# Kernel tuning notes

Hardware: AMD Instinct MI355X
Metric: run time of the kernel (lower is better)

The kernel has to match this reference:

```python
import jax, jax.numpy as jnp
import numpy as np

HIDDEN_DIM = 128
NUM_HEADS = 4
B, S = 16, 1024
NEG = -1e9
EPS = 1e-5


def setup_inputs() -> dict:
    key = jax.random.key(0)
    ks = jax.random.split(key, 6)
    D, H = HIDDEN_DIM, NUM_HEADS
    x = jax.random.normal(ks[0], (B, S, D), dtype=jnp.float32)
    edge_type_matrix = jax.random.randint(ks[1], (S, S), 0, 5, dtype=jnp.int64)
    scale = 0.02
    W_in = jax.random.normal(ks[2], (H, 3 * D, D), dtype=jnp.float32) * scale   # per-head in_proj_weight
    b_in = jax.random.normal(ks[3], (H, 3 * D), dtype=jnp.float32) * scale      # per-head in_proj_bias
    W_out = jax.random.normal(ks[4], (H, D, D), dtype=jnp.float32) * scale      # per-head out_proj.weight
    b_out = jax.random.normal(ks[5], (H, D), dtype=jnp.float32) * scale         # per-head out_proj.bias
    return {"x": x, "edge_type_matrix": edge_type_matrix,
            "W_in": W_in, "b_in": b_in, "W_out": W_out, "b_out": b_out}


def reference(x, edge_type_matrix, W_in, b_in, W_out, b_out):
    Bx, Sx, D = x.shape
    H = W_in.shape[0]
    # F.layer_norm(x, x.size()[1:]): normalize jointly over (S, D), no affine
    mu = jnp.mean(x, axis=(1, 2), keepdims=True)
    var = jnp.mean(jnp.square(x - mu), axis=(1, 2), keepdims=True)
    xn = (x - mu) / jnp.sqrt(var + EPS)
    # all heads' qkv in one contraction: [b,h,s,3D]
    qkv = jnp.einsum('bsd,hed->bhse', xn, W_in) + b_in[None, :, None, :]
    q, k, v = jnp.split(qkv, 3, axis=-1)                      # each [b,h,s,D]
    scores = jnp.einsum('bhsd,bhtd->bhst', q, k) / jnp.sqrt(jnp.float32(D))
    # additive mask per head: 0 where edge_type == head_id(1..H), else -1e9
    head_ids = jnp.arange(1, H + 1, dtype=edge_type_matrix.dtype)
    mask = jnp.where(edge_type_matrix[None, :, :] == head_ids[:, None, None],
                     jnp.float32(0.0), jnp.float32(NEG))       # [h,s,s]
    attn = jax.nn.softmax(scores + mask[None], axis=-1)
    ctx = jnp.einsum('bhst,bhtd->bhsd', attn, v)
    # torch out_proj: ctx @ W.T + b
    out_h = jnp.einsum('bhsd,hed->bhse', ctx, W_out) + b_out[None, :, None, :]
    # dropout p=0.05 is identity in eval mode; concat heads on feature dim
    out = jnp.transpose(out_h, (0, 2, 1, 3)).reshape(Bx, Sx, H * D)
    return out


if __name__ == '__main__':
    inp = setup_inputs()
    y = reference(**inp)
    print(y.shape)
```

## Files before the change

kernel.cpp:

```cpp
#include <hip/hip_runtime.h>
#include <math.h>

static constexpr int Dh = 128;
static constexpr int NH = 4;
static constexpr int NB = 16;
static constexpr int SS = 1024;
static constexpr float NEGF = -1e9f;
static constexpr float SCALE = 0.08838834764831843f;

typedef short s16x8 __attribute__((ext_vector_type(8)));
typedef short s16x4 __attribute__((ext_vector_type(4)));
typedef float f32x4 __attribute__((ext_vector_type(4)));

#define MFMA32(a, b, c) __builtin_amdgcn_mfma_f32_16x16x32_bf16(a, b, c, 0, 0, 0)
#define MFMA16(a, b, c) __builtin_amdgcn_mfma_f32_16x16x16bf16_1k(a, b, c, 0, 0, 0)

__device__ inline ushort f2bf(float f) {
    union { float f; unsigned u; } v; v.f = f;
    unsigned r = v.u + 0x7FFFu + ((v.u >> 16) & 1u);
    return (ushort)(r >> 16);
}

__global__ __launch_bounds__(256) void ln_mask_kernel(const float* __restrict__ x,
                                                      float* __restrict__ part,
                                                      const int* __restrict__ edge,
                                                      unsigned long long* __restrict__ mbit) {
    const int b = blockIdx.x >> 4, p = blockIdx.x & 15;
    const int tid = threadIdx.x;
    const float4* xb = (const float4*)(x + (size_t)b * SS * Dh) + p * 2048;
    float s = 0.f, ss = 0.f;
    for (int i = tid; i < 2048; i += 256) {
        float4 v = xb[i];
        s  += v.x + v.y + v.z + v.w;
        ss += v.x * v.x + v.y * v.y + v.z * v.z + v.w * v.w;
    }
    __shared__ float r1[256], r2[256];
    r1[tid] = s; r2[tid] = ss;
    __syncthreads();
    for (int off = 128; off > 0; off >>= 1) {
        if (tid < off) { r1[tid] += r1[tid + off]; r2[tid] += r2[tid + off]; }
        __syncthreads();
    }
    if (tid == 0) { part[blockIdx.x * 2] = r1[0]; part[blockIdx.x * 2 + 1] = r2[0]; }

    if (blockIdx.x < 64) {
        const int idx = blockIdx.x * 256 + tid;
        const int sr = idx >> 4, w = idx & 15;
        const int4* ep = (const int4*)(edge + (size_t)sr * SS + w * 64);
        unsigned long long m0 = 0, m1 = 0, m2 = 0, m3 = 0;
        #pragma unroll
        for (int j = 0; j < 16; ++j) {
            int4 e = ep[j];
            const int base = j * 4;
            m0 |= (e.x == 1) ? (1ull << (base + 0)) : 0ull;
            m1 |= (e.x == 2) ? (1ull << (base + 0)) : 0ull;
            m2 |= (e.x == 3) ? (1ull << (base + 0)) : 0ull;
            m3 |= (e.x == 4) ? (1ull << (base + 0)) : 0ull;
            m0 |= (e.y == 1) ? (1ull << (base + 1)) : 0ull;
            m1 |= (e.y == 2) ? (1ull << (base + 1)) : 0ull;
            m2 |= (e.y == 3) ? (1ull << (base + 1)) : 0ull;
            m3 |= (e.y == 4) ? (1ull << (base + 1)) : 0ull;
            m0 |= (e.z == 1) ? (1ull << (base + 2)) : 0ull;
            m1 |= (e.z == 2) ? (1ull << (base + 2)) : 0ull;
            m2 |= (e.z == 3) ? (1ull << (base + 2)) : 0ull;
            m3 |= (e.z == 4) ? (1ull << (base + 2)) : 0ull;
            m0 |= (e.w == 1) ? (1ull << (base + 3)) : 0ull;
            m1 |= (e.w == 2) ? (1ull << (base + 3)) : 0ull;
            m2 |= (e.w == 3) ? (1ull << (base + 3)) : 0ull;
            m3 |= (e.w == 4) ? (1ull << (base + 3)) : 0ull;
        }
        mbit[((size_t)0 * SS + sr) * 16 + w] = m0;
        mbit[((size_t)1 * SS + sr) * 16 + w] = m1;
        mbit[((size_t)2 * SS + sr) * 16 + w] = m2;
        mbit[((size_t)3 * SS + sr) * 16 + w] = m3;
    }
}

__global__ __launch_bounds__(256) void qkv_mfma_kernel(const float* __restrict__ x,
                                                       const float* __restrict__ w,
                                                       const float* __restrict__ bias,
                                                       const float* __restrict__ part,
                                                       ushort* __restrict__ qo,
                                                       ushort* __restrict__ ko,
                                                       ushort* __restrict__ vto) {
    __shared__ ushort smem[2 * 128 * 72];
    ushort* As = smem;
    ushort* Bs = smem + 128 * 72;
    ushort* Rs = smem;
    const int tid = threadIdx.x, wave = tid >> 6, lane = tid & 63;
    const int lrow = lane & 15, quad = lane >> 4;
    const int wm = wave & 1, wn = wave >> 1;
    const int col0 = blockIdx.x * 128;
    const int row0 = blockIdx.y * 128;
    const int bb = row0 >> 10;

    float s_ = 0.f, ss_ = 0.f;
    #pragma unroll
    for (int p = 0; p < 16; ++p) { s_ += part[(bb * 16 + p) * 2]; ss_ += part[(bb * 16 + p) * 2 + 1]; }
    const float invN = 1.0f / (float)(SS * Dh);
    const float mu = s_ * invN;
    const float rstd = 1.0f / sqrtf(ss_ * invN - mu * mu + 1e-5f);

    f32x4 acc[4][4];
    #pragma unroll
    for (int mi = 0; mi < 4; ++mi)
        #pragma unroll
        for (int ni = 0; ni < 4; ++ni) acc[mi][ni] = (f32x4){0.f, 0.f, 0.f, 0.f};

    for (int kk = 0; kk < 128; kk += 64) {
        if (kk) __syncthreads();
        #pragma unroll
        for (int p = 0; p < 8; ++p) {
            int slot = p * 256 + tid;
            int r = slot >> 4, c4 = (slot & 15) << 2;
            float4 v = *(const float4*)(x + (size_t)(row0 + r) * Dh + kk + c4);
            ushort4 pa;
            pa.x = f2bf((v.x - mu) * rstd); pa.y = f2bf((v.y - mu) * rstd);
            pa.z = f2bf((v.z - mu) * rstd); pa.w = f2bf((v.w - mu) * rstd);
            *(ushort4*)&As[r * 72 + c4] = pa;
            float4 wv = *(const float4*)(w + (size_t)(col0 + r) * Dh + kk + c4);
            ushort4 pb;
            pb.x = f2bf(wv.x); pb.y = f2bf(wv.y); pb.z = f2bf(wv.z); pb.w = f2bf(wv.w);
            *(ushort4*)&Bs[r * 72 + c4] = pb;
        }
        __syncthreads();
        #pragma unroll
        for (int kc = 0; kc < 2; ++kc) {
            s16x8 af[4], bf[4];
            #pragma unroll
            for (int mi = 0; mi < 4; ++mi)
                af[mi] = *(const s16x8*)&As[(wm * 64 + 16 * mi + lrow) * 72 + kc * 32 + quad * 8];
            #pragma unroll
            for (int ni = 0; ni < 4; ++ni)
                bf[ni] = *(const s16x8*)&Bs[(wn * 64 + 16 * ni + lrow) * 72 + kc * 32 + quad * 8];
            #pragma unroll
            for (int mi = 0; mi < 4; ++mi)
                #pragma unroll
                for (int ni = 0; ni < 4; ++ni)
                    acc[mi][ni] = MFMA32(af[mi], bf[ni], acc[mi][ni]);
        }
    }

    const int seg = col0 % 384, typ = seg >> 7, h = col0 / 384;
    const size_t bh = (size_t)bb * NH + h;
    const int sl_blk = row0 & 1023;
    float bia[4];
    #pragma unroll
    for (int ni = 0; ni < 4; ++ni) bia[ni] = bias[col0 + wn * 64 + 16 * ni + lrow];
    const float sc = (typ == 0) ? SCALE : 1.f;

    __syncthreads();
    if (typ < 2) {
        #pragma unroll
        for (int mi = 0; mi < 4; ++mi)
            #pragma unroll
            for (int ni = 0; ni < 4; ++ni)
                #pragma unroll
                for (int reg = 0; reg < 4; ++reg)
                    Rs[(wm * 64 + 16 * mi + quad * 4 + reg) * 136 + wn * 64 + 16 * ni + lrow]
                        = f2bf((acc[mi][ni][reg] + bia[ni]) * sc);
    } else {
        #pragma unroll
        for (int mi = 0; mi < 4; ++mi)
            #pragma unroll
            for (int ni = 0; ni < 4; ++ni) {
                ushort4 pk;
                pk.x = f2bf(acc[mi][ni][0] + bia[ni]);
                pk.y = f2bf(acc[mi][ni][1] + bia[ni]);
                pk.z = f2bf(acc[mi][ni][2] + bia[ni]);
                pk.w = f2bf(acc[mi][ni][3] + bia[ni]);
                *(ushort4*)&Rs[(wn * 64 + 16 * ni + lrow) * 136 + wm * 64 + 16 * mi + quad * 4] = pk;
            }
    }
    __syncthreads();

    ushort* dstb;
    int pitch;
    if (typ == 0)      { dstb = qo  + bh * SS * 128 + (size_t)sl_blk * 128; pitch = 128; }
    else if (typ == 1) { dstb = ko  + bh * SS * 128 + (size_t)sl_blk * 128; pitch = 128; }
    else               { dstb = vto + bh * (size_t)128 * SS + sl_blk;       pitch = SS;  }
    #pragma unroll
    for (int p = 0; p < 8; ++p) {
        int slot = p * 256 + tid;
        int r = slot >> 4, c8 = (slot & 15) * 8;
        *(s16x8*)&dstb[(size_t)r * pitch + c8] = *(const s16x8*)&Rs[r * 136 + c8];
    }
}

static constexpr int KS_LD = 136;
static constexpr int VT_LD = 72;
static constexpr int WS_LD = 136;
static constexpr int OS_LD = 136;
static constexpr int SMEM_N = 26112;

__global__ __launch_bounds__(256, 2) void attn_fused_kernel(const ushort* __restrict__ qg_,
                                                            const ushort* __restrict__ kg_,
                                                            const ushort* __restrict__ vg_,
                                                            const unsigned long long* __restrict__ mbit,
                                                            const float* __restrict__ wo,
                                                            const float* __restrict__ bo,
                                                            float* __restrict__ out) {
    const int bhi = blockIdx.x, qt = blockIdx.y;
    const int b = bhi >> 2, h = bhi & 3;
    const int s0 = qt * 128;
    const int tid = threadIdx.x;
    const int wave = tid >> 6, lane = tid & 63;
    const int lrow = lane & 15, quad = lane >> 4;

    __shared__ ushort smem[SMEM_N];
    ushort* Ks  = smem;
    ushort* Vt  = smem + 64 * KS_LD;
    ushort* Osl = smem + wave * 16 * OS_LD;
    ushort* Ws  = smem + 4 * 16 * OS_LD;

    const size_t bh = (size_t)(b * NH + h);
    const ushort* qg = qg_ + bh * SS * 128;
    const ushort* kg = kg_ + bh * SS * 128;
    const ushort* vg = vg_ + bh * 128 * SS;
    const unsigned long long* mrow0 = mbit + ((size_t)h * SS + (s0 + 32 * wave + lrow)) * 16;
    const unsigned long long* mrow1 = mrow0 + 16 * 16;

    s16x8 qf[2][4];
    #pragma unroll
    for (int g = 0; g < 2; ++g) {
        const ushort* qr = qg + (size_t)(s0 + 32 * wave + 16 * g + lrow) * 128 + quad * 8;
        #pragma unroll
        for (int kc = 0; kc < 4; ++kc) qf[g][kc] = *(const s16x8*)(qr + kc * 32);
    }

    s16x8 kreg[4], vreg[4];
    #pragma unroll
    for (int p = 0; p < 4; ++p) {
        int slot = p * 256 + tid;
        int r = slot >> 4, c = (slot & 15) * 8;
        kreg[p] = *(const s16x8*)(kg + (size_t)r * 128 + c);
    }
    #pragma unroll
    for (int p = 0; p < 4; ++p) {
        int slot = p * 256 + tid;
        int r = slot >> 3, c = (slot & 7) * 8;
        vreg[p] = *(const s16x8*)(vg + (size_t)r * SS + c);
    }

    f32x4 oacc[2][8];
    #pragma unroll
    for (int g = 0; g < 2; ++g)
        #pragma unroll
        for (int nb = 0; nb < 8; ++nb) oacc[g][nb] = (f32x4){0.f, 0.f, 0.f, 0.f};
    float m_run[2] = {-INFINITY, -INFINITY};
    float l_run[2] = {0.f, 0.f};

    for (int kt = 0; kt < 16; ++kt) {
        const int t0 = kt * 64;
        unsigned long long mw0 = mrow0[kt];
        unsigned long long mw1 = mrow1[kt];

        __syncthreads();
        #pragma unroll
        for (int p = 0; p < 4; ++p) {
            int slot = p * 256 + tid;
            int r = slot >> 4, c = (slot & 15) * 8;
            *(s16x8*)&Ks[r * KS_LD + c] = kreg[p];
        }
        #pragma unroll
        for (int p = 0; p < 4; ++p) {
            int slot = p * 256 + tid;
            int r = slot >> 3, c = (slot & 7) * 8;
            *(s16x8*)&Vt[r * VT_LD + c] = vreg[p];
        }
        __syncthreads();

        if (kt < 15) {
            const int t1 = t0 + 64;
            #pragma unroll
            for (int p = 0; p < 4; ++p) {
                int slot = p * 256 + tid;
                int r = slot >> 4, c = (slot & 15) * 8;
                kreg[p] = *(const s16x8*)(kg + (size_t)(t1 + r) * 128 + c);
            }
            #pragma unroll
            for (int p = 0; p < 4; ++p) {
                int slot = p * 256 + tid;
                int r = slot >> 3, c = (slot & 7) * 8;
                vreg[p] = *(const s16x8*)(vg + (size_t)r * SS + t1 + c);
            }
        }

        f32x4 sacc[2][4];
        #pragma unroll
        for (int g = 0; g < 2; ++g)
            #pragma unroll
            for (int cb = 0; cb < 4; ++cb) sacc[g][cb] = (f32x4){0.f, 0.f, 0.f, 0.f};
        #pragma unroll
        for (int cb = 0; cb < 4; ++cb) {
            s16x8 kf[4];
            #pragma unroll
            for (int kc = 0; kc < 4; ++kc)
                kf[kc] = *(const s16x8*)&Ks[(16 * cb + lrow) * KS_LD + kc * 32 + quad * 8];
            #pragma unroll
            for (int g = 0; g < 2; ++g)
                #pragma unroll
                for (int kc = 0; kc < 4; ++kc)
                    sacc[g][cb] = MFMA32(kf[kc], qf[g][kc], sacc[g][cb]);
        }

        s16x4 pf[2][4];
        #pragma unroll
        for (int g = 0; g < 2; ++g) {
            const unsigned long long mw = g ? mw1 : mw0;
            float sv[4][4];
            float tm = -INFINITY;
            #pragma unroll
            for (int cb = 0; cb < 4; ++cb) {
                unsigned nib = (unsigned)(mw >> (16 * cb + quad * 4)) & 0xFu;
                #pragma unroll
                for (int r = 0; r < 4; ++r) {
                    sv[cb][r] = (nib & (1u << r)) ? sacc[g][cb][r] : NEGF;
                    tm = fmaxf(tm, sv[cb][r]);
                }
            }
            tm = fmaxf(tm, __shfl_xor(tm, 16));
            tm = fmaxf(tm, __shfl_xor(tm, 32));
            float mn = fmaxf(m_run[g], tm);
            float al = __expf(m_run[g] - mn);
            float rs = 0.f;
            #pragma unroll
            for (int cb = 0; cb < 4; ++cb) {
                float p0 = __expf(sv[cb][0] - mn);
                float p1 = __expf(sv[cb][1] - mn);
                float p2 = __expf(sv[cb][2] - mn);
                float p3 = __expf(sv[cb][3] - mn);
                rs += (p0 + p1) + (p2 + p3);
                s16x4 pk;
                pk[0] = (short)f2bf(p0); pk[1] = (short)f2bf(p1);
                pk[2] = (short)f2bf(p2); pk[3] = (short)f2bf(p3);
                pf[g][cb] = pk;
            }
            rs += __shfl_xor(rs, 16);
            rs += __shfl_xor(rs, 32);
            l_run[g] = l_run[g] * al + rs;
            m_run[g] = mn;
            #pragma unroll
            for (int nb = 0; nb < 8; ++nb)
                #pragma unroll
                for (int r = 0; r < 4; ++r) oacc[g][nb][r] *= al;
        }

        #pragma unroll
        for (int nb = 0; nb < 8; ++nb) {
            #pragma unroll
            for (int kb = 0; kb < 4; ++kb) {
                s16x4 vf = *(const s16x4*)&Vt[(16 * nb + lrow) * VT_LD + kb * 16 + quad * 4];
                #pragma unroll
                for (int g = 0; g < 2; ++g)
                    oacc[g][nb] = MFMA16(vf, pf[g][kb], oacc[g][nb]);
            }
        }
    }

    __syncthreads();
    const float* wbase = wo + (size_t)h * Dh * Dh;
    #pragma unroll
    for (int p = 0; p < 16; ++p) {
        int slot = p * 256 + tid;
        int r = slot >> 5, c4 = (slot & 31) << 2;
        float4 wv = *(const float4*)(wbase + (size_t)r * Dh + c4);
        ushort4 pb;
        pb.x = f2bf(wv.x); pb.y = f2bf(wv.y); pb.z = f2bf(wv.z); pb.w = f2bf(wv.w);
        *(ushort4*)&Ws[r * WS_LD + c4] = pb;
    }
    s16x8 afo[2][4];
    #pragma unroll
    for (int g = 0; g < 2; ++g) {
        float inv = 1.0f / l_run[g];
        #pragma unroll
        for (int nb = 0; nb < 8; ++nb) {
            ushort4 pk;
            pk.x = f2bf(oacc[g][nb][0] * inv);
            pk.y = f2bf(oacc[g][nb][1] * inv);
            pk.z = f2bf(oacc[g][nb][2] * inv);
            pk.w = f2bf(oacc[g][nb][3] * inv);
            *(ushort4*)&Osl[lrow * OS_LD + 16 * nb + quad * 4] = pk;
        }
        #pragma unroll
        for (int kc = 0; kc < 4; ++kc)
            afo[g][kc] = *(const s16x8*)&Osl[lrow * OS_LD + kc * 32 + quad * 8];
    }
    __syncthreads();

    const size_t orow0 = (size_t)b * SS + s0 + 32 * wave;
    #pragma unroll
    for (int nb = 0; nb < 8; ++nb) {
        float bia = bo[h * Dh + nb * 16 + lrow];
        f32x4 facc[2];
        facc[0] = (f32x4){0.f, 0.f, 0.f, 0.f};
        facc[1] = (f32x4){0.f, 0.f, 0.f, 0.f};
        #pragma unroll
        for (int kc = 0; kc < 4; ++kc) {
            s16x8 wf = *(const s16x8*)&Ws[(16 * nb + lrow) * WS_LD + kc * 32 + quad * 8];
            facc[0] = MFMA32(afo[0][kc], wf, facc[0]);
            facc[1] = MFMA32(afo[1][kc], wf, facc[1]);
        }
        #pragma unroll
        for (int g = 0; g < 2; ++g)
            #pragma unroll
            for (int reg = 0; reg < 4; ++reg) {
                size_t m = orow0 + 16 * g + quad * 4 + reg;
                out[m * (NH * Dh) + h * Dh + nb * 16 + lrow] = facc[g][reg] + bia;
            }
    }
}

extern "C" void kernel_launch(void* const* d_in, const int* in_sizes, int n_in,
                              void* d_out, int out_size, void* d_ws, size_t ws_size,
                              hipStream_t stream) {
    const float* x     = (const float*)d_in[0];
    const int*   edge  = (const int*)d_in[1];
    const float* w_in  = (const float*)d_in[2];
    const float* b_in  = (const float*)d_in[3];
    const float* w_out = (const float*)d_in[4];
    const float* b_out = (const float*)d_in[5];
    float* out = (float*)d_out;

    float* ws   = (float*)d_ws;
    float* part = ws;
    unsigned long long* mbit = (unsigned long long*)(ws + 1024);
    ushort* qo  = (ushort*)(mbit + (size_t)NH * SS * 16);
    const size_t QSZ = (size_t)NB * NH * SS * 128;
    ushort* ko  = qo + QSZ;
    ushort* vto = ko + QSZ;

    ln_mask_kernel<<<256, 256, 0, stream>>>(x, part, edge, mbit);
    qkv_mfma_kernel<<<dim3(12, 128), 256, 0, stream>>>(x, w_in, b_in, part, qo, ko, vto);
    attn_fused_kernel<<<dim3(NB * NH, SS / 128), 256, 0, stream>>>(qo, ko, vto, mbit, w_out, b_out, out);
}
```

Before: 175.6 us.

## Pre-cast inputs to bf16, drop LDS staging in attention, add lazy softmax rescale

The weights and the layer-normalised x are cast to bf16 once in separate kernel passes, so the QKV GEMM loads bf16 tiles directly instead of converting on the fly. The attention kernel drops the shared-memory K/V staging and the barriers around it, and reads K and V fragments straight from global memory through the cache. Softmax now uses exp2 with log2e folded into the Q scale, and it only rescales the accumulators when the running max grows by more than a threshold. The out-projection runs from registers, and the block order is remapped across XCDs to improve L2 locality. The extra kernel launch and the bf16 staging buffers add overhead, and the direct global K/V reads may raise memory latency.

```diff
diff --git a/kernel.cpp b/kernel.cpp
--- a/kernel.cpp
+++ b/kernel.cpp
@@ -7,6 +7,7 @@
 static constexpr int SS = 1024;
 static constexpr float NEGF = -1e9f;
 static constexpr float SCALE = 0.08838834764831843f;
+static constexpr float LOG2E = 1.4426950408889634f;
 
 typedef short s16x8 __attribute__((ext_vector_type(8)));
 typedef short s16x4 __attribute__((ext_vector_type(4)));
@@ -24,13 +25,17 @@
 __global__ __launch_bounds__(256) void ln_mask_kernel(const float* __restrict__ x,
                                                       float* __restrict__ part,
                                                       const int* __restrict__ edge,
-                                                      unsigned long long* __restrict__ mbit) {
+                                                      unsigned long long* __restrict__ mbit,
+                                                      const float* __restrict__ w_in,
+                                                      const float* __restrict__ w_out,
+                                                      ushort* __restrict__ wb,
+                                                      ushort* __restrict__ wob) {
     const int b = blockIdx.x >> 4, p = blockIdx.x & 15;
     const int tid = threadIdx.x;
-    const float4* xb = (const float4*)(x + (size_t)b * SS * Dh) + p * 2048;
+    const float4* xb4 = (const float4*)(x + (size_t)b * SS * Dh) + p * 2048;
     float s = 0.f, ss = 0.f;
     for (int i = tid; i < 2048; i += 256) {
-        float4 v = xb[i];
+        float4 v = xb4[i];
         s  += v.x + v.y + v.z + v.w;
         ss += v.x * v.x + v.y * v.y + v.z * v.z + v.w * v.w;
     }
@@ -73,13 +78,53 @@
         mbit[((size_t)1 * SS + sr) * 16 + w] = m1;
         mbit[((size_t)2 * SS + sr) * 16 + w] = m2;
         mbit[((size_t)3 * SS + sr) * 16 + w] = m3;
-    }
-}
-
-__global__ __launch_bounds__(256) void qkv_mfma_kernel(const float* __restrict__ x,
-                                                       const float* __restrict__ w,
+    } else if (blockIdx.x < 160) {
+        const int slot = (blockIdx.x - 64) * 256 + tid;
+        const float4* sp = (const float4*)w_in + (size_t)slot * 2;
+        float4 a = sp[0], c = sp[1];
+        s16x8 pk;
+        pk[0] = (short)f2bf(a.x); pk[1] = (short)f2bf(a.y);
+        pk[2] = (short)f2bf(a.z); pk[3] = (short)f2bf(a.w);
+        pk[4] = (short)f2bf(c.x); pk[5] = (short)f2bf(c.y);
+        pk[6] = (short)f2bf(c.z); pk[7] = (short)f2bf(c.w);
+        *(s16x8*)(wb + (size_t)slot * 8) = pk;
+    } else if (blockIdx.x < 192) {
+        const int slot = (blockIdx.x - 160) * 256 + tid;
+        const float4* sp = (const float4*)w_out + (size_t)slot * 2;
+        float4 a = sp[0], c = sp[1];
+        s16x8 pk;
+        pk[0] = (short)f2bf(a.x); pk[1] = (short)f2bf(a.y);
+        pk[2] = (short)f2bf(a.z); pk[3] = (short)f2bf(a.w);
+        pk[4] = (short)f2bf(c.x); pk[5] = (short)f2bf(c.y);
+        pk[6] = (short)f2bf(c.z); pk[7] = (short)f2bf(c.w);
+        *(s16x8*)(wob + (size_t)slot * 8) = pk;
+    }
+}
+
+__global__ __launch_bounds__(256) void xcast_kernel(const float* __restrict__ x,
+                                                    const float* __restrict__ part,
+                                                    ushort* __restrict__ xb) {
+    const int b = blockIdx.x >> 6;
+    float s = 0.f, ss = 0.f;
+    #pragma unroll
+    for (int p = 0; p < 16; ++p) { s += part[(b * 16 + p) * 2]; ss += part[(b * 16 + p) * 2 + 1]; }
+    const float invN = 1.0f / (float)(SS * Dh);
+    const float mu = s * invN;
+    const float rstd = 1.0f / sqrtf(ss * invN - mu * mu + 1e-5f);
+    const size_t base = ((size_t)blockIdx.x * 256 + threadIdx.x) * 8;
+    float4 v0 = *(const float4*)(x + base);
+    float4 v1 = *(const float4*)(x + base + 4);
+    s16x8 pk;
+    pk[0] = (short)f2bf((v0.x - mu) * rstd); pk[1] = (short)f2bf((v0.y - mu) * rstd);
+    pk[2] = (short)f2bf((v0.z - mu) * rstd); pk[3] = (short)f2bf((v0.w - mu) * rstd);
+    pk[4] = (short)f2bf((v1.x - mu) * rstd); pk[5] = (short)f2bf((v1.y - mu) * rstd);
+    pk[6] = (short)f2bf((v1.z - mu) * rstd); pk[7] = (short)f2bf((v1.w - mu) * rstd);
+    *(s16x8*)(xb + base) = pk;
+}
+
+__global__ __launch_bounds__(256) void qkv_mfma_kernel(const ushort* __restrict__ xb,
+                                                       const ushort* __restrict__ wb,
                                                        const float* __restrict__ bias,
-                                                       const float* __restrict__ part,
                                                        ushort* __restrict__ qo,
                                                        ushort* __restrict__ ko,
                                                        ushort* __restrict__ vto) {
@@ -94,13 +139,6 @@
     const int row0 = blockIdx.y * 128;
     const int bb = row0 >> 10;
 
-    float s_ = 0.f, ss_ = 0.f;
-    #pragma unroll
-    for (int p = 0; p < 16; ++p) { s_ += part[(bb * 16 + p) * 2]; ss_ += part[(bb * 16 + p) * 2 + 1]; }
-    const float invN = 1.0f / (float)(SS * Dh);
-    const float mu = s_ * invN;
-    const float rstd = 1.0f / sqrtf(ss_ * invN - mu * mu + 1e-5f);
-
     f32x4 acc[4][4];
     #pragma unroll
     for (int mi = 0; mi < 4; ++mi)
@@ -110,18 +148,11 @@
     for (int kk = 0; kk < 128; kk += 64) {
         if (kk) __syncthreads();
         #pragma unroll
-        for (int p = 0; p < 8; ++p) {
+        for (int p = 0; p < 4; ++p) {
             int slot = p * 256 + tid;
-            int r = slot >> 4, c4 = (slot & 15) << 2;
-            float4 v = *(const float4*)(x + (size_t)(row0 + r) * Dh + kk + c4);
-            ushort4 pa;
-            pa.x = f2bf((v.x - mu) * rstd); pa.y = f2bf((v.y - mu) * rstd);
-            pa.z = f2bf((v.z - mu) * rstd); pa.w = f2bf((v.w - mu) * rstd);
-            *(ushort4*)&As[r * 72 + c4] = pa;
-            float4 wv = *(const float4*)(w + (size_t)(col0 + r) * Dh + kk + c4);
-            ushort4 pb;
-            pb.x = f2bf(wv.x); pb.y = f2bf(wv.y); pb.z = f2bf(wv.z); pb.w = f2bf(wv.w);
-            *(ushort4*)&Bs[r * 72 + c4] = pb;
+            int r = slot >> 3, c8 = (slot & 7) * 8;
+            *(s16x8*)&As[r * 72 + c8] = *(const s16x8*)(xb + (size_t)(row0 + r) * Dh + kk + c8);
+            *(s16x8*)&Bs[r * 72 + c8] = *(const s16x8*)(wb + (size_t)(col0 + r) * Dh + kk + c8);
         }
         __syncthreads();
         #pragma unroll
@@ -147,7 +178,7 @@
     float bia[4];
     #pragma unroll
     for (int ni = 0; ni < 4; ++ni) bia[ni] = bias[col0 + wn * 64 + 16 * ni + lrow];
-    const float sc = (typ == 0) ? SCALE : 1.f;
+    const float sc = (typ == 0) ? SCALE * LOG2E : 1.f;
 
     __syncthreads();
     if (typ < 2) {
@@ -187,36 +218,27 @@
     }
 }
 
-static constexpr int KS_LD = 136;
-static constexpr int VT_LD = 72;
-static constexpr int WS_LD = 136;
-static constexpr int OS_LD = 136;
-static constexpr int SMEM_N = 26112;
-
 __global__ __launch_bounds__(256, 2) void attn_fused_kernel(const ushort* __restrict__ qg_,
                                                             const ushort* __restrict__ kg_,
                                                             const ushort* __restrict__ vg_,
                                                             const unsigned long long* __restrict__ mbit,
-                                                            const float* __restrict__ wo,
+                                                            const ushort* __restrict__ wob,
                                                             const float* __restrict__ bo,
                                                             float* __restrict__ out) {
-    const int bhi = blockIdx.x, qt = blockIdx.y;
+    const int id = blockIdx.x;
+    const int xcd = id & 7, rr = id >> 3;
+    const int qt = rr & 7, bhg = rr >> 3;
+    const int bhi = (bhg << 3) | xcd;
     const int b = bhi >> 2, h = bhi & 3;
     const int s0 = qt * 128;
     const int tid = threadIdx.x;
     const int wave = tid >> 6, lane = tid & 63;
     const int lrow = lane & 15, quad = lane >> 4;
 
-    __shared__ ushort smem[SMEM_N];
-    ushort* Ks  = smem;
-    ushort* Vt  = smem + 64 * KS_LD;
-    ushort* Osl = smem + wave * 16 * OS_LD;
-    ushort* Ws  = smem + 4 * 16 * OS_LD;
-
     const size_t bh = (size_t)(b * NH + h);
     const ushort* qg = qg_ + bh * SS * 128;
     const ushort* kg = kg_ + bh * SS * 128;
-    const ushort* vg = vg_ + bh * 128 * SS;
+    const ushort* vg = vg_ + bh * (size_t)128 * SS;
     const unsigned long long* mrow0 = mbit + ((size_t)h * SS + (s0 + 32 * wave + lrow)) * 16;
     const unsigned long long* mrow1 = mrow0 + 16 * 16;
 
@@ -226,20 +248,6 @@
         const ushort* qr = qg + (size_t)(s0 + 32 * wave + 16 * g + lrow) * 128 + quad * 8;
         #pragma unroll
         for (int kc = 0; kc < 4; ++kc) qf[g][kc] = *(const s16x8*)(qr + kc * 32);
-    }
-
-    s16x8 kreg[4], vreg[4];
-    #pragma unroll
-    for (int p = 0; p < 4; ++p) {
-        int slot = p * 256 + tid;
-        int r = slot >> 4, c = (slot & 15) * 8;
-        kreg[p] = *(const s16x8*)(kg + (size_t)r * 128 + c);
-    }
-    #pragma unroll
-    for (int p = 0; p < 4; ++p) {
-        int slot = p * 256 + tid;
-        int r = slot >> 3, c = (slot & 7) * 8;
-        vreg[p] = *(const s16x8*)(vg + (size_t)r * SS + c);
     }
 
     f32x4 oacc[2][8];
@@ -252,39 +260,8 @@
 
     for (int kt = 0; kt < 16; ++kt) {
         const int t0 = kt * 64;
-        unsigned long long mw0 = mrow0[kt];
-        unsigned long long mw1 = mrow1[kt];
-
-        __syncthreads();
-        #pragma unroll
-        for (int p = 0; p < 4; ++p) {
-            int slot = p * 256 + tid;
-            int r = slot >> 4, c = (slot & 15) * 8;
-            *(s16x8*)&Ks[r * KS_LD + c] = kreg[p];
-        }
-        #pragma unroll
-        for (int p = 0; p < 4; ++p) {
-            int slot = p * 256 + tid;
-            int r = slot >> 3, c = (slot & 7) * 8;
-            *(s16x8*)&Vt[r * VT_LD + c] = vreg[p];
-        }
-        __syncthreads();
-
-        if (kt < 15) {
-            const int t1 = t0 + 64;
-            #pragma unroll
-            for (int p = 0; p < 4; ++p) {
-                int slot = p * 256 + tid;
-                int r = slot >> 4, c = (slot & 15) * 8;
-                kreg[p] = *(const s16x8*)(kg + (size_t)(t1 + r) * 128 + c);
-            }
-            #pragma unroll
-            for (int p = 0; p < 4; ++p) {
-                int slot = p * 256 + tid;
-                int r = slot >> 3, c = (slot & 7) * 8;
-                vreg[p] = *(const s16x8*)(vg + (size_t)r * SS + t1 + c);
-            }
-        }
+        const unsigned long long mw0 = mrow0[kt];
+        const unsigned long long mw1 = mrow1[kt];
 
         f32x4 sacc[2][4];
         #pragma unroll
@@ -294,14 +271,14 @@
         #pragma unroll
         for (int cb = 0; cb < 4; ++cb) {
             s16x8 kf[4];
-            #pragma unroll
-            for (int kc = 0; kc < 4; ++kc)
-                kf[kc] = *(const s16x8*)&Ks[(16 * cb + lrow) * KS_LD + kc * 32 + quad * 8];
-            #pragma unroll
-            for (int g = 0; g < 2; ++g)
-                #pragma unroll
-                for (int kc = 0; kc < 4; ++kc)
-                    sacc[g][cb] = MFMA32(kf[kc], qf[g][kc], sacc[g][cb]);
+            const ushort* kr = kg + (size_t)(t0 + 16 * cb + lrow) * 128 + quad * 8;
+            #pragma unroll
+            for (int kc = 0; kc < 4; ++kc) kf[kc] = *(const s16x8*)(kr + kc * 32);
+            #pragma unroll
+            for (int kc = 0; kc < 4; ++kc) {
+                sacc[0][cb] = MFMA32(kf[kc], qf[0][kc], sacc[0][cb]);
+                sacc[1][cb] = MFMA32(kf[kc], qf[1][kc], sacc[1][cb]);
+            }
         }
 
         s16x4 pf[2][4];
@@ -321,15 +298,24 @@
             }
             tm = fmaxf(tm, __shfl_xor(tm, 16));
             tm = fmaxf(tm, __shfl_xor(tm, 32));
-            float mn = fmaxf(m_run[g], tm);
-            float al = __expf(m_run[g] - mn);
+            float mn = m_run[g];
+            if (!__all(tm <= mn + 12.f)) {
+                mn = fmaxf(mn, tm);
+                float al = __builtin_amdgcn_exp2f(m_run[g] - mn);
+                l_run[g] *= al;
+                #pragma unroll
+                for (int nb = 0; nb < 8; ++nb)
+                    #pragma unroll
+                    for (int r = 0; r < 4; ++r) oacc[g][nb][r] *= al;
+                m_run[g] = mn;
+            }
             float rs = 0.f;
             #pragma unroll
             for (int cb = 0; cb < 4; ++cb) {
-                float p0 = __expf(sv[cb][0] - mn);
-                float p1 = __expf(sv[cb][1] - mn);
-                float p2 = __expf(sv[cb][2] - mn);
-                float p3 = __expf(sv[cb][3] - mn);
+                float p0 = __builtin_amdgcn_exp2f(sv[cb][0] - mn);
+                float p1 = __builtin_amdgcn_exp2f(sv[cb][1] - mn);
+                float p2 = __builtin_amdgcn_exp2f(sv[cb][2] - mn);
+                float p3 = __builtin_amdgcn_exp2f(sv[cb][3] - mn);
                 rs += (p0 + p1) + (p2 + p3);
                 s16x4 pk;
                 pk[0] = (short)f2bf(p0); pk[1] = (short)f2bf(p1);
@@ -338,75 +324,56 @@
             }
             rs += __shfl_xor(rs, 16);
             rs += __shfl_xor(rs, 32);
-            l_run[g] = l_run[g] * al + rs;
-            m_run[g] = mn;
-            #pragma unroll
-            for (int nb = 0; nb < 8; ++nb)
-                #pragma unroll
-                for (int r = 0; r < 4; ++r) oacc[g][nb][r] *= al;
+            l_run[g] += rs;
         }
 
         #pragma unroll
         for (int nb = 0; nb < 8; ++nb) {
+            const ushort* vr = vg + (size_t)(16 * nb + lrow) * SS + t0 + quad * 4;
             #pragma unroll
             for (int kb = 0; kb < 4; ++kb) {
-                s16x4 vf = *(const s16x4*)&Vt[(16 * nb + lrow) * VT_LD + kb * 16 + quad * 4];
-                #pragma unroll
-                for (int g = 0; g < 2; ++g)
-                    oacc[g][nb] = MFMA16(vf, pf[g][kb], oacc[g][nb]);
-            }
-        }
-    }
-
-    __syncthreads();
-    const float* wbase = wo + (size_t)h * Dh * Dh;
-    #pragma unroll
-    for (int p = 0; p < 16; ++p) {
-        int slot = p * 256 + tid;
-        int r = slot >> 5, c4 = (slot & 31) << 2;
-        float4 wv = *(const float4*)(wbase + (size_t)r * Dh + c4);
-        ushort4 pb;
-        pb.x = f2bf(wv.x); pb.y = f2bf(wv.y); pb.z = f2bf(wv.z); pb.w = f2bf(wv.w);
-        *(ushort4*)&Ws[r * WS_LD + c4] = pb;
-    }
-    s16x8 afo[2][4];
+                s16x4 vf = *(const s16x4*)(vr + kb * 16);
+                oacc[0][nb] = MFMA16(vf, pf[0][kb], oacc[0][nb]);
+                oacc[1][nb] = MFMA16(vf, pf[1][kb], oacc[1][nb]);
+            }
+        }
+    }
+
+    s16x4 aO[2][8];
     #pragma unroll
     for (int g = 0; g < 2; ++g) {
         float inv = 1.0f / l_run[g];
         #pragma unroll
         for (int nb = 0; nb < 8; ++nb) {
-            ushort4 pk;
-            pk.x = f2bf(oacc[g][nb][0] * inv);
-            pk.y = f2bf(oacc[g][nb][1] * inv);
-            pk.z = f2bf(oacc[g][nb][2] * inv);
-            pk.w = f2bf(oacc[g][nb][3] * inv);
-            *(ushort4*)&Osl[lrow * OS_LD + 16 * nb + quad * 4] = pk;
-        }
-        #pragma unroll
-        for (int kc = 0; kc < 4; ++kc)
-            afo[g][kc] = *(const s16x8*)&Osl[lrow * OS_LD + kc * 32 + quad * 8];
-    }
-    __syncthreads();
-
+            s16x4 pk;
+            pk[0] = (short)f2bf(oacc[g][nb][0] * inv);
+            pk[1] = (short)f2bf(oacc[g][nb][1] * inv);
+            pk[2] = (short)f2bf(oacc[g][nb][2] * inv);
+            pk[3] = (short)f2bf(oacc[g][nb][3] * inv);
+            aO[g][nb] = pk;
+        }
+    }
+    const ushort* wbh = wob + (size_t)h * Dh * Dh;
     const size_t orow0 = (size_t)b * SS + s0 + 32 * wave;
     #pragma unroll
-    for (int nb = 0; nb < 8; ++nb) {
-        float bia = bo[h * Dh + nb * 16 + lrow];
+    for (int eb = 0; eb < 8; ++eb) {
+        float bia = bo[h * Dh + eb * 16 + lrow];
         f32x4 facc[2];
         facc[0] = (f32x4){0.f, 0.f, 0.f, 0.f};
         facc[1] = (f32x4){0.f, 0.f, 0.f, 0.f};
-        #pragma unroll
-        for (int kc = 0; kc < 4; ++kc) {
-            s16x8 wf = *(const s16x8*)&Ws[(16 * nb + lrow) * WS_LD + kc * 32 + quad * 8];
-            facc[0] = MFMA32(afo[0][kc], wf, facc[0]);
-            facc[1] = MFMA32(afo[1][kc], wf, facc[1]);
+        const ushort* wr = wbh + (size_t)(eb * 16 + lrow) * Dh + quad * 4;
+        #pragma unroll
+        for (int nb = 0; nb < 8; ++nb) {
+            s16x4 wf = *(const s16x4*)(wr + nb * 16);
+            facc[0] = MFMA16(aO[0][nb], wf, facc[0]);
+            facc[1] = MFMA16(aO[1][nb], wf, facc[1]);
         }
         #pragma unroll
         for (int g = 0; g < 2; ++g)
             #pragma unroll
             for (int reg = 0; reg < 4; ++reg) {
                 size_t m = orow0 + 16 * g + quad * 4 + reg;
-                out[m * (NH * Dh) + h * Dh + nb * 16 + lrow] = facc[g][reg] + bia;
+                out[m * (NH * Dh) + h * Dh + eb * 16 + lrow] = facc[g][reg] + bia;
             }
     }
 }
@@ -429,8 +396,12 @@
     const size_t QSZ = (size_t)NB * NH * SS * 128;
     ushort* ko  = qo + QSZ;
     ushort* vto = ko + QSZ;
-
-    ln_mask_kernel<<<256, 256, 0, stream>>>(x, part, edge, mbit);
-    qkv_mfma_kernel<<<dim3(12, 128), 256, 0, stream>>>(x, w_in, b_in, part, qo, ko, vto);
-    attn_fused_kernel<<<dim3(NB * NH, SS / 128), 256, 0, stream>>>(qo, ko, vto, mbit, w_out, b_out, out);
-}
+    ushort* xb  = vto + QSZ;
+    ushort* wb  = xb + (size_t)NB * SS * Dh;
+    ushort* wob = wb + (size_t)NH * 3 * Dh * Dh;
+
+    ln_mask_kernel<<<256, 256, 0, stream>>>(x, part, edge, mbit, w_in, w_out, wb, wob);
+    xcast_kernel<<<1024, 256, 0, stream>>>(x, part, xb);
+    qkv_mfma_kernel<<<dim3(12, 128), 256, 0, stream>>>(xb, wb, b_in, qo, ko, vto);
+    attn_fused_kernel<<<512, 256, 0, stream>>>(qo, ko, vto, mbit, wob, b_out, out);
+}
```

After: 294.3 us. 1.68x slower.
